# Kernel tuning notes

Hardware: AMD Instinct MI355X
Metric: run time of the kernel (lower is better)

## Reference

```python
import jax, jax.numpy as jnp
import numpy as np

PI = 3.14159  # literal used by the original module
N_QUBITS = 3
N_LAYERS = 2


def _apply_ry(state, theta, wire):
    """Apply RY(theta) on `wire`. state: (B, 2, 2, 2). theta: scalar or (B,)."""
    st = jnp.moveaxis(state, wire + 1, -1)
    c = jnp.cos(theta * 0.5)
    s = jnp.sin(theta * 0.5)
    nd = st.ndim - 1  # rank of st[..., 0]
    c = c.reshape(c.shape + (1,) * (nd - c.ndim))
    s = s.reshape(s.shape + (1,) * (nd - s.ndim))
    s0, s1 = st[..., 0], st[..., 1]
    st = jnp.stack([c * s0 - s * s1, s * s0 + c * s1], axis=-1)
    return jnp.moveaxis(st, -1, wire + 1)


def _apply_cnot(state, ctrl, tgt):
    """CNOT with control `ctrl`, target `tgt`: flip target where control=1."""
    st = jnp.moveaxis(state, (ctrl + 1, tgt + 1), (-2, -1))
    st = jnp.stack([st[..., 0, :], st[..., 1, ::-1]], axis=-2)
    return jnp.moveaxis(st, (-2, -1), (ctrl + 1, tgt + 1))


def _circuit(x, weights):
    B = x.shape[0]
    dt = x.dtype
    # |000...0> initial state, batched: (B, 2, 2, 2)
    state = jnp.zeros((B,) + (2,) * N_QUBITS, dt)
    state = state.at[(slice(None),) + (0,) * N_QUBITS].set(1.0)
    # angle encoding: RY(x[:, i] * pi) on wire i
    for i in range(N_QUBITS):
        state = _apply_ry(state, x[:, i] * PI, i)
    # variational layers: RY(weights[l, i]) then CNOT chain
    for l in range(N_LAYERS):
        for i in range(N_QUBITS):
            state = _apply_ry(state, weights[l, i], i)
        for i in range(N_QUBITS - 1):
            state = _apply_cnot(state, i, i + 1)
    # <Z_i> = sum_s |amp_s|^2 * (1 - 2*bit_i(s))  (RY/CNOT keep state real)
    probs = (state * state).reshape(B, 2 ** N_QUBITS)
    idx = jnp.arange(2 ** N_QUBITS)
    bits = (idx[None, :] >> (N_QUBITS - 1 - jnp.arange(N_QUBITS)[:, None])) & 1
    signs = (1.0 - 2.0 * bits).astype(dt)  # (n_qubits, 8)
    return probs @ signs.T  # (B, n_qubits)


def setup_inputs() -> dict:
    key = jax.random.key(0)
    k1, k2 = jax.random.split(key)
    x = jax.random.normal(k1, (2097152, 4), jnp.float32)
    weights = jax.random.normal(k2, (2, 3), jnp.float32) * 0.1
    return {"x": x, "weights": weights}


def reference(x, weights):
    return _circuit(x, weights)
```

## Files before the change

### kernel.cpp

```cpp
#include <hip/hip_runtime.h>


__global__ __launch_bounds__(256) void qfl_kernel(
    const float4* __restrict__ x, const float* __restrict__ w,
    float* __restrict__ out, int n)
{
    __shared__ float sout[1536];
    const int tid = threadIdx.x;
    const long long base = (long long)blockIdx.x * 512;

    const float hw0 = 0.5f * w[0], hw1 = 0.5f * w[1], hw2 = 0.5f * w[2];
    const float c3 = __cosf(0.5f * w[3]), s3 = __sinf(0.5f * w[3]);
    const float c4 = __cosf(0.5f * w[4]), s4 = __sinf(0.5f * w[4]);
    const float c5 = __cosf(0.5f * w[5]), s5 = __sinf(0.5f * w[5]);

    const float HPI = 0.5f * 3.14159f;

    #pragma unroll
    for (int half = 0; half < 2; ++half) {
        const long long e = base + half * 256 + tid;
        float4 xv = (e < (long long)n) ? x[e] : make_float4(0.f, 0.f, 0.f, 0.f);

        float ta = fmaf(xv.x, HPI, hw0);
        float tb = fmaf(xv.y, HPI, hw1);
        float tc = fmaf(xv.z, HPI, hw2);
        float a0 = __cosf(ta), a1 = __sinf(ta);
        float b0 = __cosf(tb), b1 = __sinf(tb);
        float c0 = __cosf(tc), c1 = __sinf(tc);

        float a0b0 = a0 * b0, a0b1 = a0 * b1, a1b0 = a1 * b0, a1b1 = a1 * b1;
        float v0 = a0b0 * c0, v1 = a0b0 * c1;
        float v2 = a0b1 * c1, v3 = a0b1 * c0;
        float v4 = a1b1 * c0, v5 = a1b1 * c1;
        float v6 = a1b0 * c1, v7 = a1b0 * c0;

        { float u, v;
          u = v0; v = v4; v0 = c3*u - s3*v; v4 = s3*u + c3*v;
          u = v1; v = v5; v1 = c3*u - s3*v; v5 = s3*u + c3*v;
          u = v2; v = v6; v2 = c3*u - s3*v; v6 = s3*u + c3*v;
          u = v3; v = v7; v3 = c3*u - s3*v; v7 = s3*u + c3*v; }
        { float u, v;
          u = v0; v = v2; v0 = c4*u - s4*v; v2 = s4*u + c4*v;
          u = v1; v = v3; v1 = c4*u - s4*v; v3 = s4*u + c4*v;
          u = v4; v = v6; v4 = c4*u - s4*v; v6 = s4*u + c4*v;
          u = v5; v = v7; v5 = c4*u - s4*v; v7 = s4*u + c4*v; }
        { float u, v;
          u = v0; v = v1; v0 = c5*u - s5*v; v1 = s5*u + c5*v;
          u = v2; v = v3; v2 = c5*u - s5*v; v3 = s5*u + c5*v;
          u = v4; v = v5; v4 = c5*u - s5*v; v5 = s5*u + c5*v;
          u = v6; v = v7; v6 = c5*u - s5*v; v7 = s5*u + c5*v; }

        float q0 = v0*v0, q1 = v1*v1, q2 = v2*v2, q3 = v3*v3;
        float q4 = v4*v4, q5 = v5*v5, q6 = v6*v6, q7 = v7*v7;
        float o0 = (q0 + q1 + q2 + q3) - (q4 + q5 + q6 + q7);
        float o1 = (q0 + q1 + q6 + q7) - (q2 + q3 + q4 + q5);
        float o2 = (q0 + q3 + q5 + q6) - (q1 + q2 + q4 + q7);

        sout[half * 768 + 3 * tid + 0] = o0;
        sout[half * 768 + 3 * tid + 1] = o1;
        sout[half * 768 + 3 * tid + 2] = o2;
    }
    __syncthreads();

    const long long T  = (long long)n * 3;
    const long long t2 = T >> 1;
    const long long b2 = (long long)blockIdx.x * 768;
    const float2* s2 = (const float2*)sout;
    float2* og = (float2*)out;
    #pragma unroll
    for (int k = 0; k < 3; ++k) {
        long long idx = b2 + k * 256 + tid;
        if (idx < t2) og[idx] = s2[k * 256 + tid];
    }
    if ((T & 1) && tid == 0 && blockIdx.x == gridDim.x - 1) {
        out[T - 1] = sout[T - 1 - (long long)blockIdx.x * 1536];
    }
}

extern "C" void kernel_launch(void* const* d_in, const int* in_sizes, int n_in,
                              void* d_out, int out_size, void* d_ws, size_t ws_size,
                              hipStream_t stream) {
    const float4* x = (const float4*)d_in[0];
    const float*  w = (const float*)d_in[1];
    float* out = (float*)d_out;
    int n = in_sizes[0] / 4;
    int blocks = (n + 511) / 512;
    qfl_kernel<<<blocks, 256, 0, stream>>>(x, w, out, n);
}
```

Before: 81.80 us.

## Process four rows per thread, use raw hardware sin/cos, vectorize stores

Each thread now handles four rows, with all four float4 loads issued up front, and blocks cover 1024 rows, so the grid is halved. The trig calls switch to the amdgcn sin/cos builtins, which take their argument in revolutions, so the angle constants are pre-scaled by 1/(4*pi) to skip range reduction. Full blocks take a bounds-free path that loads without checks and writes out with float4 stores. The cost is more registers per thread and a dependence on how accurate the hardware sin/cos is.

```diff
diff --git a/kernel.cpp b/kernel.cpp
--- a/kernel.cpp
+++ b/kernel.cpp
@@ -1,79 +1,101 @@
 #include <hip/hip_runtime.h>
 
+
+__device__ __forceinline__ void qfl_row(
+    float4 xv,
+    float hw0, float hw1, float hw2,
+    float c3, float s3, float c4, float s4, float c5, float s5,
+    float& o0, float& o1, float& o2)
+{
+    const float XS = 0.24999948f;
+    float ta = fmaf(xv.x, XS, hw0);
+    float tb = fmaf(xv.y, XS, hw1);
+    float tc = fmaf(xv.z, XS, hw2);
+    float a0 = __builtin_amdgcn_cosf(ta), a1 = __builtin_amdgcn_sinf(ta);
+    float b0 = __builtin_amdgcn_cosf(tb), b1 = __builtin_amdgcn_sinf(tb);
+    float c0 = __builtin_amdgcn_cosf(tc), c1 = __builtin_amdgcn_sinf(tc);
+
+    float a0b0 = a0 * b0, a0b1 = a0 * b1, a1b0 = a1 * b0, a1b1 = a1 * b1;
+    float v0 = a0b0 * c0, v1 = a0b0 * c1;
+    float v2 = a0b1 * c1, v3 = a0b1 * c0;
+    float v4 = a1b1 * c0, v5 = a1b1 * c1;
+    float v6 = a1b0 * c1, v7 = a1b0 * c0;
+
+    { float u, v;
+      u = v0; v = v4; v0 = c3*u - s3*v; v4 = s3*u + c3*v;
+      u = v1; v = v5; v1 = c3*u - s3*v; v5 = s3*u + c3*v;
+      u = v2; v = v6; v2 = c3*u - s3*v; v6 = s3*u + c3*v;
+      u = v3; v = v7; v3 = c3*u - s3*v; v7 = s3*u + c3*v; }
+    { float u, v;
+      u = v0; v = v2; v0 = c4*u - s4*v; v2 = s4*u + c4*v;
+      u = v1; v = v3; v1 = c4*u - s4*v; v3 = s4*u + c4*v;
+      u = v4; v = v6; v4 = c4*u - s4*v; v6 = s4*u + c4*v;
+      u = v5; v = v7; v5 = c4*u - s4*v; v7 = s4*u + c4*v; }
+    { float u, v;
+      u = v0; v = v1; v0 = c5*u - s5*v; v1 = s5*u + c5*v;
+      u = v2; v = v3; v2 = c5*u - s5*v; v3 = s5*u + c5*v;
+      u = v4; v = v5; v4 = c5*u - s5*v; v5 = s5*u + c5*v;
+      u = v6; v = v7; v6 = c5*u - s5*v; v7 = s5*u + c5*v; }
+
+    float q0 = v0*v0, q1 = v1*v1, q2 = v2*v2, q3 = v3*v3;
+    float q4 = v4*v4, q5 = v5*v5, q6 = v6*v6, q7 = v7*v7;
+    float e01 = q0 + q1, e23 = q2 + q3, e45 = q4 + q5, e67 = q6 + q7;
+    o0 = (e01 + e23) - (e45 + e67);
+    o1 = (e01 + e67) - (e23 + e45);
+    o2 = (q0 + q3 + q5 + q6) - (q1 + q2 + q4 + q7);
+}
 
 __global__ __launch_bounds__(256) void qfl_kernel(
     const float4* __restrict__ x, const float* __restrict__ w,
     float* __restrict__ out, int n)
 {
-    __shared__ float sout[1536];
-    const int tid = threadIdx.x;
-    const long long base = (long long)blockIdx.x * 512;
+    __shared__ float sout[3072];
+    const int tid  = threadIdx.x;
+    const int base = blockIdx.x * 1024;
 
-    const float hw0 = 0.5f * w[0], hw1 = 0.5f * w[1], hw2 = 0.5f * w[2];
-    const float c3 = __cosf(0.5f * w[3]), s3 = __sinf(0.5f * w[3]);
-    const float c4 = __cosf(0.5f * w[4]), s4 = __sinf(0.5f * w[4]);
-    const float c5 = __cosf(0.5f * w[5]), s5 = __sinf(0.5f * w[5]);
+    const float R = 0.07957747155f;
+    const float hw0 = w[0] * R, hw1 = w[1] * R, hw2 = w[2] * R;
+    const float t3 = w[3] * R, t4 = w[4] * R, t5 = w[5] * R;
+    const float c3 = __builtin_amdgcn_cosf(t3), s3 = __builtin_amdgcn_sinf(t3);
+    const float c4 = __builtin_amdgcn_cosf(t4), s4 = __builtin_amdgcn_sinf(t4);
+    const float c5 = __builtin_amdgcn_cosf(t5), s5 = __builtin_amdgcn_sinf(t5);
 
-    const float HPI = 0.5f * 3.14159f;
+    const bool full = (base + 1024 <= n);
+
+    float4 xv[4];
+    if (full) {
+        #pragma unroll
+        for (int h = 0; h < 4; ++h) xv[h] = x[base + h * 256 + tid];
+    } else {
+        #pragma unroll
+        for (int h = 0; h < 4; ++h) {
+            int e = base + h * 256 + tid;
+            xv[h] = (e < n) ? x[e] : make_float4(0.f, 0.f, 0.f, 0.f);
+        }
+    }
 
     #pragma unroll
-    for (int half = 0; half < 2; ++half) {
-        const long long e = base + half * 256 + tid;
-        float4 xv = (e < (long long)n) ? x[e] : make_float4(0.f, 0.f, 0.f, 0.f);
-
-        float ta = fmaf(xv.x, HPI, hw0);
-        float tb = fmaf(xv.y, HPI, hw1);
-        float tc = fmaf(xv.z, HPI, hw2);
-        float a0 = __cosf(ta), a1 = __sinf(ta);
-        float b0 = __cosf(tb), b1 = __sinf(tb);
-        float c0 = __cosf(tc), c1 = __sinf(tc);
-
-        float a0b0 = a0 * b0, a0b1 = a0 * b1, a1b0 = a1 * b0, a1b1 = a1 * b1;
-        float v0 = a0b0 * c0, v1 = a0b0 * c1;
-        float v2 = a0b1 * c1, v3 = a0b1 * c0;
-        float v4 = a1b1 * c0, v5 = a1b1 * c1;
-        float v6 = a1b0 * c1, v7 = a1b0 * c0;
-
-        { float u, v;
-          u = v0; v = v4; v0 = c3*u - s3*v; v4 = s3*u + c3*v;
-          u = v1; v = v5; v1 = c3*u - s3*v; v5 = s3*u + c3*v;
-          u = v2; v = v6; v2 = c3*u - s3*v; v6 = s3*u + c3*v;
-          u = v3; v = v7; v3 = c3*u - s3*v; v7 = s3*u + c3*v; }
-        { float u, v;
-          u = v0; v = v2; v0 = c4*u - s4*v; v2 = s4*u + c4*v;
-          u = v1; v = v3; v1 = c4*u - s4*v; v3 = s4*u + c4*v;
-          u = v4; v = v6; v4 = c4*u - s4*v; v6 = s4*u + c4*v;
-          u = v5; v = v7; v5 = c4*u - s4*v; v7 = s4*u + c4*v; }
-        { float u, v;
-          u = v0; v = v1; v0 = c5*u - s5*v; v1 = s5*u + c5*v;
-          u = v2; v = v3; v2 = c5*u - s5*v; v3 = s5*u + c5*v;
-          u = v4; v = v5; v4 = c5*u - s5*v; v5 = s5*u + c5*v;
-          u = v6; v = v7; v6 = c5*u - s5*v; v7 = s5*u + c5*v; }
-
-        float q0 = v0*v0, q1 = v1*v1, q2 = v2*v2, q3 = v3*v3;
-        float q4 = v4*v4, q5 = v5*v5, q6 = v6*v6, q7 = v7*v7;
-        float o0 = (q0 + q1 + q2 + q3) - (q4 + q5 + q6 + q7);
-        float o1 = (q0 + q1 + q6 + q7) - (q2 + q3 + q4 + q5);
-        float o2 = (q0 + q3 + q5 + q6) - (q1 + q2 + q4 + q7);
-
-        sout[half * 768 + 3 * tid + 0] = o0;
-        sout[half * 768 + 3 * tid + 1] = o1;
-        sout[half * 768 + 3 * tid + 2] = o2;
+    for (int h = 0; h < 4; ++h) {
+        float o0, o1, o2;
+        qfl_row(xv[h], hw0, hw1, hw2, c3, s3, c4, s4, c5, s5, o0, o1, o2);
+        sout[h * 768 + 3 * tid + 0] = o0;
+        sout[h * 768 + 3 * tid + 1] = o1;
+        sout[h * 768 + 3 * tid + 2] = o2;
     }
     __syncthreads();
 
-    const long long T  = (long long)n * 3;
-    const long long t2 = T >> 1;
-    const long long b2 = (long long)blockIdx.x * 768;
-    const float2* s2 = (const float2*)sout;
-    float2* og = (float2*)out;
-    #pragma unroll
-    for (int k = 0; k < 3; ++k) {
-        long long idx = b2 + k * 256 + tid;
-        if (idx < t2) og[idx] = s2[k * 256 + tid];
-    }
-    if ((T & 1) && tid == 0 && blockIdx.x == gridDim.x - 1) {
-        out[T - 1] = sout[T - 1 - (long long)blockIdx.x * 1536];
+    if (full) {
+        const float4* s4p = (const float4*)sout;
+        float4* og = (float4*)out + (long long)blockIdx.x * 768;
+        #pragma unroll
+        for (int k = 0; k < 3; ++k) og[k * 256 + tid] = s4p[k * 256 + tid];
+    } else {
+        const long long T  = (long long)n * 3;
+        const long long b0 = (long long)base * 3;
+        for (int k = tid; k < 3072; k += 256) {
+            long long idx = b0 + k;
+            if (idx < T) out[idx] = sout[k];
+        }
     }
 }
 
@@ -84,6 +106,6 @@
     const float*  w = (const float*)d_in[1];
     float* out = (float*)d_out;
     int n = in_sizes[0] / 4;
-    int blocks = (n + 511) / 512;
+    int blocks = (n + 1023) / 1024;
     qfl_kernel<<<blocks, 256, 0, stream>>>(x, w, out, n);
 }
```

Result: no change. 81.86 us (+0.1%).
